# Performance work log

Measured on AMD Instinct MI355X. Metric: run time of the kernel, lower is better.

The kernel has to match this reference:

```python
import jax, jax.numpy as jnp
import numpy as np

SQRT5 = 2.2360679774997896


def setup_inputs() -> dict:
    key = jax.random.key(0)
    k1, k2, k3 = jax.random.split(key, 3)
    n, m, d = 1024, 1024, 8
    X1 = jax.random.normal(k1, (n, d), dtype=jnp.float32)
    X2 = jax.random.normal(k2, (m, d), dtype=jnp.float32)
    c = jnp.asarray(1.0, dtype=jnp.float32)  # overall_scaling (scalar param)
    # character_length: positive lengthscales per feature
    l = 0.5 + jax.random.uniform(k3, (d,), dtype=jnp.float32)
    return {"X1": X1, "X2": X2, "c": c, "l": l}


def reference(X1, X2, c, l):
    # X1: [n, d], X2: [m, d] -> out [n, d, m, d]
    d = l.shape[0]
    inv_l2 = 1.0 / (l * l)                       # [d]
    DX1X2 = X1[:, None, :] - X2[None, :, :]      # [n, m, d]
    # scaled pairwise distance r[i,j] = || (X1_i - X2_j) / l ||
    r = jnp.sqrt(jnp.sum((DX1X2 / l) ** 2, axis=-1))   # [n, m]
    fr = (5.0 / 3.0) * jnp.exp(-SQRT5 * r)             # [n, m]
    # M[a,b] = (1/l^2) * eye(d) with column-wise broadcast (matches torch):
    M = inv_l2 * jnp.eye(d, dtype=l.dtype)             # [d, d], diag = 1/l^2
    A = fr * (1.0 + SQRT5 * r)                         # [n, m]
    D = DX1X2 * inv_l2                                 # [n, m, d]
    # k[i,a,j,b] = A[i,j]*M[a,b] - 5*fr[i,j]*D[i,j,a]*D[i,j,b]
    k = jnp.einsum('ij,ab->iajb', A, M) - 5.0 * jnp.einsum('ij,ija,ijb->iajb', fr, D, D)
    return (c * c) * k
```

## Files before the change

kernel.cpp:

```cpp
#include <hip/hip_runtime.h>

#define SQRT5F 2.2360679774997896f


__global__ __launch_bounds__(256) void deriv2_matern52_kernel(
    const float* __restrict__ X1,
    const float* __restrict__ X2,
    const float* __restrict__ c_ptr,
    const float* __restrict__ l_ptr,
    float* __restrict__ out,
    int m )
{
    const int t  = threadIdx.x;
    const int h  = t & 1;
    const int p  = t >> 1;

    const int bid = blockIdx.x;
    const int a   = bid & 7;
    const int i   = bid >> 3;

    const float c  = c_ptr[0];
    const float c2 = c * c;

    float inv_l2[8];
#pragma unroll
    for (int k = 0; k < 8; ++k) {
        const float lv = l_ptr[k];
        inv_l2[k] = 1.0f / (lv * lv);
    }

    float asel[8];
#pragma unroll
    for (int k = 0; k < 8; ++k) asel[k] = (k == a) ? 1.0f : 0.0f;

    float il_a = 0.0f;
#pragma unroll
    for (int k = 0; k < 8; ++k) il_a = fmaf(asel[k], inv_l2[k], il_a);

    float dk[4];
#pragma unroll
    for (int k = 0; k < 4; ++k)
        dk[k] = (((a & 3) == k) && ((a >> 2) == h)) ? 1.0f : 0.0f;

    const float4 x1a = ((const float4*)(X1 + (size_t)i * 8))[0];
    const float4 x1b = ((const float4*)(X1 + (size_t)i * 8))[1];
    const float x1v[8] = { x1a.x, x1a.y, x1a.z, x1a.w,
                           x1b.x, x1b.y, x1b.z, x1b.w };

    float* op = out + (size_t)bid * (size_t)m * 8 + (size_t)t * 4;
    const float* xp = X2 + (size_t)p * 8;

    for (int s = 0; s < m; s += 128) {
        const float4 x2a = ((const float4*)xp)[0];
        const float4 x2b = ((const float4*)xp)[1];
        const float x2v[8] = { x2a.x, x2a.y, x2a.z, x2a.w,
                               x2b.x, x2b.y, x2b.z, x2b.w };

        float D[8];
        float r2 = 0.0f;
#pragma unroll
        for (int k = 0; k < 8; ++k) {
            const float dx = x1v[k] - x2v[k];
            D[k] = dx * inv_l2[k];
            r2 += dx * D[k];
        }

        const float r  = sqrtf(r2);
        const float fr = (5.0f / 3.0f) * expf(-SQRT5F * r);
        const float A  = fr * (1.0f + SQRT5F * r);

        const float Acil = A * c2 * il_a;
        const float cf   = -5.0f * fr * c2;

        float Da = 0.0f;
#pragma unroll
        for (int k = 0; k < 8; ++k) Da = fmaf(asel[k], D[k], Da);
        const float Dca = cf * Da;

        float v[4];
#pragma unroll
        for (int k = 0; k < 4; ++k) {
            const float Db = h ? D[4 + k] : D[k];
            v[k] = fmaf(dk[k], Acil, Dca * Db);
        }

        *(float4*)op = make_float4(v[0], v[1], v[2], v[3]);

        op += 128 * 8;
        xp += 128 * 8;
    }
}

extern "C" void kernel_launch(void* const* d_in, const int* in_sizes, int n_in,
                              void* d_out, int out_size, void* d_ws, size_t ws_size,
                              hipStream_t stream) {
    const float* X1 = (const float*)d_in[0];
    const float* X2 = (const float*)d_in[1];
    const float* c  = (const float*)d_in[2];
    const float* l  = (const float*)d_in[3];
    float* out = (float*)d_out;

    const int d = in_sizes[3];
    const int n = in_sizes[0] / d;
    const int m = in_sizes[1] / d;

    dim3 grid(n * 8);
    dim3 block(256);
    deriv2_matern52_kernel<<<grid, block, 0, stream>>>(X1, X2, c, l, out, m);
}
```

Baseline: 269.8 us.

## Remap grid to persistent blocks over j-tiles, striding rows of X1

Each block now owns a fixed 128-column tile of X2 and one output feature a, then loops over rows i with a grid stride. The launch shrinks from n*8 blocks to jbn*8*16. X2 is loaded once per thread, and the c2*il_a and -5*c2 factors are hoisted out of the loop. The intent is to cut block launch overhead and redundant X2 loads in this write-bound kernel. The risk is fewer blocks (1024) and strided output writes across loop iterations, which may reduce memory-level parallelism.

```diff
diff --git a/kernel.cpp b/kernel.cpp
--- a/kernel.cpp
+++ b/kernel.cpp
@@ -9,15 +9,23 @@
     const float* __restrict__ c_ptr,
     const float* __restrict__ l_ptr,
     float* __restrict__ out,
-    int m )
+    int m ,
+    int n )
 {
-    const int t  = threadIdx.x;
-    const int h  = t & 1;
-    const int p  = t >> 1;
+    const int t = threadIdx.x;
+    const int h = t & 1;
+    const int p = t >> 1;
 
     const int bid = blockIdx.x;
-    const int a   = bid & 7;
-    const int i   = bid >> 3;
+    const int G   = gridDim.x;
+
+    const int jbn   = m >> 7;
+    const int jb    = bid % jbn;
+    const int a     = (bid / jbn) & 7;
+    const int i0    = bid / (jbn * 8);
+    const int istep = G / (jbn * 8);
+
+    const int j = (jb << 7) + p;
 
     const float c  = c_ptr[0];
     const float c2 = c * c;
@@ -42,19 +50,23 @@
     for (int k = 0; k < 4; ++k)
         dk[k] = (((a & 3) == k) && ((a >> 2) == h)) ? 1.0f : 0.0f;
 
-    const float4 x1a = ((const float4*)(X1 + (size_t)i * 8))[0];
-    const float4 x1b = ((const float4*)(X1 + (size_t)i * 8))[1];
-    const float x1v[8] = { x1a.x, x1a.y, x1a.z, x1a.w,
-                           x1b.x, x1b.y, x1b.z, x1b.w };
+    const float4 x2a = ((const float4*)(X2 + (size_t)j * 8))[0];
+    const float4 x2b = ((const float4*)(X2 + (size_t)j * 8))[1];
+    const float x2v[8] = { x2a.x, x2a.y, x2a.z, x2a.w,
+                           x2b.x, x2b.y, x2b.z, x2b.w };
 
-    float* op = out + (size_t)bid * (size_t)m * 8 + (size_t)t * 4;
-    const float* xp = X2 + (size_t)p * 8;
+    const float c2il = c2 * il_a;
+    const float m5c2 = -5.0f * c2;
 
-    for (int s = 0; s < m; s += 128) {
-        const float4 x2a = ((const float4*)xp)[0];
-        const float4 x2b = ((const float4*)xp)[1];
-        const float x2v[8] = { x2a.x, x2a.y, x2a.z, x2a.w,
-                               x2b.x, x2b.y, x2b.z, x2b.w };
+    float* op = out + ((size_t)(i0 * 8 + a) * (size_t)m + (size_t)(jb << 7)) * 8
+                    + (size_t)t * 4;
+    const size_t ostep = (size_t)istep * 8 * (size_t)m * 8;
+
+    for (int i = i0; i < n; i += istep, op += ostep) {
+        const float4 x1a = ((const float4*)(X1 + (size_t)i * 8))[0];
+        const float4 x1b = ((const float4*)(X1 + (size_t)i * 8))[1];
+        const float x1v[8] = { x1a.x, x1a.y, x1a.z, x1a.w,
+                               x1b.x, x1b.y, x1b.z, x1b.w };
 
         float D[8];
         float r2 = 0.0f;
@@ -65,12 +77,10 @@
             r2 += dx * D[k];
         }
 
-        const float r  = sqrtf(r2);
-        const float fr = (5.0f / 3.0f) * expf(-SQRT5F * r);
-        const float A  = fr * (1.0f + SQRT5F * r);
-
-        const float Acil = A * c2 * il_a;
-        const float cf   = -5.0f * fr * c2;
+        const float r    = sqrtf(r2);
+        const float fr   = (5.0f / 3.0f) * expf(-SQRT5F * r);
+        const float Acil = fr * (1.0f + SQRT5F * r) * c2il;
+        const float cf   = m5c2 * fr;
 
         float Da = 0.0f;
 #pragma unroll
@@ -85,9 +95,6 @@
         }
 
         *(float4*)op = make_float4(v[0], v[1], v[2], v[3]);
-
-        op += 128 * 8;
-        xp += 128 * 8;
     }
 }
 
@@ -104,7 +111,10 @@
     const int n = in_sizes[0] / d;
     const int m = in_sizes[1] / d;
 
-    dim3 grid(n * 8);
+    const int jbn = m >> 7;
+    int G = jbn * 8 * 16;
+    if (G / (jbn * 8) > n) G = jbn * 8 * n;
+    dim3 grid(G);
     dim3 block(256);
-    deriv2_matern52_kernel<<<grid, block, 0, stream>>>(X1, X2, c, l, out, m);
+    deriv2_matern52_kernel<<<grid, block, 0, stream>>>(X1, X2, c, l, out, m, n);
 }
```

New measurement: 285.1 us. +5.7%, slower.
